# Performance work log

Measured on AMD Instinct MI355X. Metric: run time of the kernel, lower is better.

The kernel has to match this reference:

```python
import jax, jax.numpy as jnp
import numpy as np


def setup_inputs() -> dict:
    key = jax.random.key(0)
    ks = jax.random.split(key, 5)
    B, S, H = 4, 4096, 512
    std = 1.0 / np.sqrt(H)
    x = jax.random.normal(ks[0], (B, S, H), dtype=jnp.float32)
    relative_pos = jax.random.normal(ks[1], (B, S, H), dtype=jnp.float32)
    Wq = jax.random.normal(ks[2], (H, H), dtype=jnp.float32) * std
    Wk = jax.random.normal(ks[3], (H, H), dtype=jnp.float32) * std
    Wv = jax.random.normal(ks[4], (H, H), dtype=jnp.float32) * std
    bq = jnp.zeros((H,), dtype=jnp.float32)
    bk = jnp.zeros((H,), dtype=jnp.float32)
    bv = jnp.zeros((H,), dtype=jnp.float32)
    return {"x": x, "relative_pos": relative_pos, "Wq": Wq, "bq": bq,
            "Wk": Wk, "bk": bk, "Wv": Wv, "bv": bv}


def reference(x, relative_pos, Wq, bq, Wk, bk, Wv, bv):
    H = x.shape[-1]
    scale = jnp.sqrt(jnp.asarray(H, dtype=x.dtype))
    # torch Linear: y = x @ W^T + b
    Q = jnp.einsum('bsh,oh->bso', x, Wq) + bq
    K = jnp.einsum('bsh,oh->bso', x, Wk) + bk
    V = jnp.einsum('bsh,oh->bso', x, Wv) + bv
    Kr = jnp.einsum('bsh,oh->bso', relative_pos, Wk) + bk
    # two score terms, each [B,S,S]
    scores = (jnp.einsum('bqd,bkd->bqk', Q, K) +
              jnp.einsum('bqd,bkd->bqk', Q, Kr)) / scale
    weights = jax.nn.softmax(scores, axis=-1)
    return jnp.einsum('bqk,bkd->bqd', weights, V)
```

## Files before the change

### kernel.cpp

```cpp
#include <hip/hip_runtime.h>
#include <stdint.h>

typedef __attribute__((ext_vector_type(8))) short bf16x8;
typedef __attribute__((ext_vector_type(4))) float f32x4;

#define AS1 __attribute__((address_space(1)))
#define AS3 __attribute__((address_space(3)))

__device__ __forceinline__ void gl2lds16(const void* g, void* l) {
    __builtin_amdgcn_global_load_lds((const AS1 void*)g, (AS3 void*)l, 16, 0, 0);
}

__device__ __forceinline__ unsigned short f2bf(float f) {
    uint32_t u = __builtin_bit_cast(uint32_t, f);
    uint32_t r = (u + 0x7fffu + ((u >> 16) & 1u)) >> 16;
    return (unsigned short)r;
}

constexpr int S = 4096;
constexpr int H = 512;
constexpr size_t OFF_XB  = 0;
constexpr size_t OFF_SB  = 16777216;
constexpr size_t OFF_WQB = 33554432;
constexpr size_t OFF_WKB = 34078720;
constexpr size_t OFF_WVB = 34603008;
constexpr size_t OFF_BQK = 35127296;
constexpr size_t OFF_QB  = 35131392;
constexpr size_t OFF_K2B = OFF_QB  + 16777216;
constexpr size_t OFF_VTB = OFF_K2B + 16777216;
constexpr size_t OFF_PB  = OFF_VTB + 16777216;
constexpr size_t OFF_L   = OFF_PB  + 134217728;

__global__ __launch_bounds__(256) void prep_x(const float* __restrict__ x,
                                              const float* __restrict__ rp,
                                              unsigned short* __restrict__ xb,
                                              unsigned short* __restrict__ sb) {
    const int i = (blockIdx.x * 256 + threadIdx.x) * 4;
    float4 xv = *(const float4*)(x + i);
    float4 rv = *(const float4*)(rp + i);
    uint2 xo, so;
    xo.x = (uint32_t)f2bf(xv.x) | ((uint32_t)f2bf(xv.y) << 16);
    xo.y = (uint32_t)f2bf(xv.z) | ((uint32_t)f2bf(xv.w) << 16);
    so.x = (uint32_t)f2bf(xv.x + rv.x) | ((uint32_t)f2bf(xv.y + rv.y) << 16);
    so.y = (uint32_t)f2bf(xv.z + rv.z) | ((uint32_t)f2bf(xv.w + rv.w) << 16);
    *(uint2*)(xb + i) = xo;
    *(uint2*)(sb + i) = so;
}

__global__ __launch_bounds__(256) void prep_w(const float* __restrict__ wq,
                                              const float* __restrict__ wk,
                                              const float* __restrict__ wv,
                                              const float* __restrict__ bq,
                                              const float* __restrict__ bk,
                                              unsigned short* __restrict__ wqb,
                                              unsigned short* __restrict__ wkb,
                                              unsigned short* __restrict__ wvb,
                                              float* __restrict__ bqk,
                                              float* __restrict__ lrow) {
    const int t = blockIdx.x * 256 + threadIdx.x;
    const int i = t * 4;
    float4 q = *(const float4*)(wq + i);
    float4 k = *(const float4*)(wk + i);
    float4 v = *(const float4*)(wv + i);
    uint2 o;
    o.x = (uint32_t)f2bf(q.x) | ((uint32_t)f2bf(q.y) << 16);
    o.y = (uint32_t)f2bf(q.z) | ((uint32_t)f2bf(q.w) << 16);
    *(uint2*)(wqb + i) = o;
    o.x = (uint32_t)f2bf(k.x) | ((uint32_t)f2bf(k.y) << 16);
    o.y = (uint32_t)f2bf(k.z) | ((uint32_t)f2bf(k.w) << 16);
    *(uint2*)(wkb + i) = o;
    o.x = (uint32_t)f2bf(v.x) | ((uint32_t)f2bf(v.y) << 16);
    o.y = (uint32_t)f2bf(v.z) | ((uint32_t)f2bf(v.w) << 16);
    *(uint2*)(wvb + i) = o;
    if (t < 128) {
        *(float4*)(bqk + t * 4) = *(const float4*)(bq + t * 4);
    } else if (t < 256) {
        const int u = t - 128;
        float4 b = *(const float4*)(bk + u * 4);
        *(float4*)(bqk + 512 + u * 4) = make_float4(2.f * b.x, 2.f * b.y, 2.f * b.z, 2.f * b.w);
    }
    if (t < 4096) {
        *(float4*)(lrow + t * 4) = make_float4(0.f, 0.f, 0.f, 0.f);
    }
}

template <int MODE, int SWZ>
__global__ __launch_bounds__(256, 2)
void gemm_bt(const unsigned short* __restrict__ Abase,
             const unsigned short* __restrict__ Bbase,
             void* __restrict__ Cbase,
             int M, int N, int K,
             long long sAz, long long sBz, long long sCz,
             const float* __restrict__ bias_n, long long sBNz,
             const float* __restrict__ bias_m,
             float scale,
             float* __restrict__ rowdiv, long long sRz)
{
    int bx = blockIdx.x, by = blockIdx.y, bz = blockIdx.z;
    if (SWZ) {
        const int gx = gridDim.x, gy = gridDim.y;
        const int id  = bx + gx * (by + gridDim.y * bz);
        const int xcd = id & 7;
        const int k   = id >> 3;
        const int kg  = k / gx;
        bx = k - kg * gx;
        const int g = xcd + 8 * kg;
        const int gz = g / gy;
        by = g - gz * gy;
        bz = gz;
    }
    const int z = bz;
    const unsigned short* A  = Abase + (size_t)z * (size_t)sAz;
    const unsigned short* Bm = Bbase + (size_t)z * (size_t)sBz;
    const int bn = bx * 128;
    const int bm = by * 128;

    constexpr int SMEM_BYTES = (MODE == 2) ? (128 * 136 * 2) : (4 * 4096 * 2);
    __shared__ __align__(16) char smem[SMEM_BYTES];
    unsigned short* As = (unsigned short*)smem;
    unsigned short* Bs = (unsigned short*)(smem + 16384);

    const int tid  = threadIdx.x;
    const int wave = tid >> 6;
    const int lane = tid & 63;
    const int lm   = lane & 15;
    const int quad = lane >> 4;
    const int wm   = (wave >> 1) * 64;
    const int wn   = (wave & 1) * 64;

    const int r0 = tid >> 2;
    const int p0 = tid & 3;

    f32x4 acc[4][4] = {};

    for (int k0 = 0; k0 < K; k0 += 64) {
        __syncthreads();
        #pragma unroll
        for (int pp = 0; pp < 2; pp++) {
            const unsigned short* Ap = A  + (size_t)(bm + r0) * K + k0 + pp * 32 + p0 * 8;
            const unsigned short* Bp = Bm + (size_t)(bn + r0) * K + k0 + pp * 32 + p0 * 8;
            unsigned short* Asp = As + pp * 4096;
            unsigned short* Bsp = Bs + pp * 4096;
            gl2lds16(Ap,                    Asp + wave * 512);
            gl2lds16(Ap + (size_t)64 * K,   Asp + 2048 + wave * 512);
            gl2lds16(Bp,                    Bsp + wave * 512);
            gl2lds16(Bp + (size_t)64 * K,   Bsp + 2048 + wave * 512);
        }
        __syncthreads();

        #pragma unroll
        for (int pp = 0; pp < 2; pp++) {
            bf16x8 af[4], bfr[4];
            #pragma unroll
            for (int t = 0; t < 4; t++)
                af[t]  = *(const bf16x8*)(As + pp * 4096 + (wm + t * 16 + lm) * 32 + quad * 8);
            #pragma unroll
            for (int t = 0; t < 4; t++)
                bfr[t] = *(const bf16x8*)(Bs + pp * 4096 + (wn + t * 16 + lm) * 32 + quad * 8);
            #pragma unroll
            for (int mt = 0; mt < 4; mt++)
                #pragma unroll
                for (int nt = 0; nt < 4; nt++)
                    acc[mt][nt] = __builtin_amdgcn_mfma_f32_16x16x32_bf16(af[mt], bfr[nt], acc[mt][nt], 0, 0, 0);
        }
    }

    if (MODE == 0) {
        unsigned short* C = (unsigned short*)Cbase + (size_t)z * (size_t)sCz;
        const float* bn_ptr = bias_n ? bias_n + (size_t)z * (size_t)sBNz : nullptr;
        #pragma unroll
        for (int mt = 0; mt < 4; mt++) {
            #pragma unroll
            for (int i = 0; i < 4; i++) {
                const int row = bm + wm + mt * 16 + quad * 4 + i;
                const float badd = bias_m ? bias_m[row] : 0.0f;
                const size_t rb = (size_t)row * (size_t)N;
                #pragma unroll
                for (int nt = 0; nt < 4; nt++) {
                    const int col = bn + wn + nt * 16 + lm;
                    float v = acc[mt][nt][i] * scale + badd;
                    if (bn_ptr) v += bn_ptr[col];
                    C[rb + col] = f2bf(v);
                }
            }
        }
    } else if (MODE == 1) {
        float* C = (float*)Cbase + (size_t)z * (size_t)sCz;
        const float* rd = rowdiv + (size_t)z * (size_t)sRz;
        #pragma unroll
        for (int mt = 0; mt < 4; mt++) {
            #pragma unroll
            for (int i = 0; i < 4; i++) {
                const int row = bm + wm + mt * 16 + quad * 4 + i;
                const float inv = 1.0f / rd[row];
                const size_t rb = (size_t)row * (size_t)N;
                #pragma unroll
                for (int nt = 0; nt < 4; nt++) {
                    const int col = bn + wn + nt * 16 + lm;
                    C[rb + col] = acc[mt][nt][i] * inv;
                }
            }
        }
    } else {
        unsigned short* C = (unsigned short*)Cbase + (size_t)z * (size_t)sCz;
        float* lr = rowdiv + (size_t)z * (size_t)sRz;
        unsigned short* Ct = (unsigned short*)smem;
        __syncthreads();
        #pragma unroll
        for (int mt = 0; mt < 4; mt++) {
            #pragma unroll
            for (int i = 0; i < 4; i++) {
                const int r = wm + mt * 16 + quad * 4 + i;
                float rsum = 0.f;
                #pragma unroll
                for (int nt = 0; nt < 4; nt++) {
                    float p = __expf(acc[mt][nt][i] * scale);
                    rsum += p;
                    Ct[r * 136 + wn + nt * 16 + lm] = f2bf(p);
                }
                rsum += __shfl_xor(rsum, 1);
                rsum += __shfl_xor(rsum, 2);
                rsum += __shfl_xor(rsum, 4);
                rsum += __shfl_xor(rsum, 8);
                if (lm == 0) atomicAdd(lr + bm + r, rsum);
            }
        }
        __syncthreads();
        #pragma unroll
        for (int j = 0; j < 8; j++) {
            const int r   = (tid >> 4) + 16 * j;
            const int c16 = tid & 15;
            uint4 vv = *(const uint4*)(Ct + r * 136 + c16 * 8);
            *(uint4*)(C + (size_t)(bm + r) * (size_t)N + bn + c16 * 8) = vv;
        }
    }
}

extern "C" void kernel_launch(void* const* d_in, const int* in_sizes, int n_in,
                              void* d_out, int out_size, void* d_ws, size_t ws_size,
                              hipStream_t stream) {
    const float* x  = (const float*)d_in[0];
    const float* rp = (const float*)d_in[1];
    const float* Wq = (const float*)d_in[2];
    const float* bq = (const float*)d_in[3];
    const float* Wk = (const float*)d_in[4];
    const float* bk = (const float*)d_in[5];
    const float* Wv = (const float*)d_in[6];
    const float* bv = (const float*)d_in[7];

    char* ws = (char*)d_ws;
    unsigned short* xb  = (unsigned short*)(ws + OFF_XB);
    unsigned short* sb  = (unsigned short*)(ws + OFF_SB);
    unsigned short* wqb = (unsigned short*)(ws + OFF_WQB);
    unsigned short* wkb = (unsigned short*)(ws + OFF_WKB);
    unsigned short* wvb = (unsigned short*)(ws + OFF_WVB);
    float*          bqk = (float*)(ws + OFF_BQK);
    unsigned short* qb  = (unsigned short*)(ws + OFF_QB);
    unsigned short* k2b = (unsigned short*)(ws + OFF_K2B);
    unsigned short* vtb = (unsigned short*)(ws + OFF_VTB);
    unsigned short* pb  = (unsigned short*)(ws + OFF_PB);
    float*          lrow = (float*)(ws + OFF_L);

    prep_x<<<8192, 256, 0, stream>>>(x, rp, xb, sb);
    prep_w<<<256, 256, 0, stream>>>(Wq, Wk, Wv, bq, bk, wqb, wkb, wvb, bqk, lrow);

    gemm_bt<0, 1><<<dim3(4, 128, 2), 256, 0, stream>>>(
        xb, wqb, qb, 16384, 512, 512,
        8388608, 262144, 8388608,
        bqk, 512, nullptr, 1.0f, nullptr, 0);
    gemm_bt<0, 0><<<dim3(32, 4, 4), 256, 0, stream>>>(
        wvb, xb, vtb, 512, 4096, 512,
        0, (long long)S * H, (long long)S * H,
        nullptr, 0, bv, 1.0f, nullptr, 0);
    gemm_bt<2, 0><<<dim3(32, 32, 4), 256, 0, stream>>>(
        qb, k2b, pb, 4096, 4096, 512,
        (long long)S * H, (long long)S * H, (long long)S * S,
        nullptr, 0, nullptr, 0.044194173824159216f,
        lrow, 4096);
    gemm_bt<1, 1><<<dim3(4, 32, 4), 256, 0, stream>>>(
        pb, vtb, d_out, 4096, 512, 4096,
        (long long)S * S, (long long)S * H, (long long)S * H,
        nullptr, 0, nullptr, 1.0f, lrow, 4096);
}
```

Measured before the change: 347.5 us.

## Merge prep kernels, stage MODE-0 output via LDS, deepen PV K-panels

The two preprocessing kernels are merged into one launch that branches on block index. The projection GEMM epilogue (MODE 0) now writes its bf16 tile through LDS and stores coalesced 16-byte rows instead of scattered 2-byte stores. The final P·V GEMM loads four 32-wide K panels per sync instead of two, halving barrier count over its long K=4096 loop. The price is a larger LDS footprint for the PV kernel, which can limit occupancy.

```diff
diff --git a/kernel.cpp b/kernel.cpp
--- a/kernel.cpp
+++ b/kernel.cpp
@@ -31,60 +31,61 @@
 constexpr size_t OFF_PB  = OFF_VTB + 16777216;
 constexpr size_t OFF_L   = OFF_PB  + 134217728;
 
-__global__ __launch_bounds__(256) void prep_x(const float* __restrict__ x,
-                                              const float* __restrict__ rp,
-                                              unsigned short* __restrict__ xb,
-                                              unsigned short* __restrict__ sb) {
-    const int i = (blockIdx.x * 256 + threadIdx.x) * 4;
-    float4 xv = *(const float4*)(x + i);
-    float4 rv = *(const float4*)(rp + i);
-    uint2 xo, so;
-    xo.x = (uint32_t)f2bf(xv.x) | ((uint32_t)f2bf(xv.y) << 16);
-    xo.y = (uint32_t)f2bf(xv.z) | ((uint32_t)f2bf(xv.w) << 16);
-    so.x = (uint32_t)f2bf(xv.x + rv.x) | ((uint32_t)f2bf(xv.y + rv.y) << 16);
-    so.y = (uint32_t)f2bf(xv.z + rv.z) | ((uint32_t)f2bf(xv.w + rv.w) << 16);
-    *(uint2*)(xb + i) = xo;
-    *(uint2*)(sb + i) = so;
-}
-
-__global__ __launch_bounds__(256) void prep_w(const float* __restrict__ wq,
-                                              const float* __restrict__ wk,
-                                              const float* __restrict__ wv,
-                                              const float* __restrict__ bq,
-                                              const float* __restrict__ bk,
-                                              unsigned short* __restrict__ wqb,
-                                              unsigned short* __restrict__ wkb,
-                                              unsigned short* __restrict__ wvb,
-                                              float* __restrict__ bqk,
-                                              float* __restrict__ lrow) {
-    const int t = blockIdx.x * 256 + threadIdx.x;
-    const int i = t * 4;
-    float4 q = *(const float4*)(wq + i);
-    float4 k = *(const float4*)(wk + i);
-    float4 v = *(const float4*)(wv + i);
-    uint2 o;
-    o.x = (uint32_t)f2bf(q.x) | ((uint32_t)f2bf(q.y) << 16);
-    o.y = (uint32_t)f2bf(q.z) | ((uint32_t)f2bf(q.w) << 16);
-    *(uint2*)(wqb + i) = o;
-    o.x = (uint32_t)f2bf(k.x) | ((uint32_t)f2bf(k.y) << 16);
-    o.y = (uint32_t)f2bf(k.z) | ((uint32_t)f2bf(k.w) << 16);
-    *(uint2*)(wkb + i) = o;
-    o.x = (uint32_t)f2bf(v.x) | ((uint32_t)f2bf(v.y) << 16);
-    o.y = (uint32_t)f2bf(v.z) | ((uint32_t)f2bf(v.w) << 16);
-    *(uint2*)(wvb + i) = o;
-    if (t < 128) {
-        *(float4*)(bqk + t * 4) = *(const float4*)(bq + t * 4);
-    } else if (t < 256) {
-        const int u = t - 128;
-        float4 b = *(const float4*)(bk + u * 4);
-        *(float4*)(bqk + 512 + u * 4) = make_float4(2.f * b.x, 2.f * b.y, 2.f * b.z, 2.f * b.w);
-    }
-    if (t < 4096) {
-        *(float4*)(lrow + t * 4) = make_float4(0.f, 0.f, 0.f, 0.f);
-    }
-}
-
-template <int MODE, int SWZ>
+__global__ __launch_bounds__(256) void prep_all(const float* __restrict__ x,
+                                                const float* __restrict__ rp,
+                                                const float* __restrict__ wq,
+                                                const float* __restrict__ wk,
+                                                const float* __restrict__ wv,
+                                                const float* __restrict__ bq,
+                                                const float* __restrict__ bk,
+                                                unsigned short* __restrict__ xb,
+                                                unsigned short* __restrict__ sb,
+                                                unsigned short* __restrict__ wqb,
+                                                unsigned short* __restrict__ wkb,
+                                                unsigned short* __restrict__ wvb,
+                                                float* __restrict__ bqk,
+                                                float* __restrict__ lrow) {
+    if (blockIdx.x < 8192) {
+        const int i = (blockIdx.x * 256 + threadIdx.x) * 4;
+        float4 xv = *(const float4*)(x + i);
+        float4 rv = *(const float4*)(rp + i);
+        uint2 xo, so;
+        xo.x = (uint32_t)f2bf(xv.x) | ((uint32_t)f2bf(xv.y) << 16);
+        xo.y = (uint32_t)f2bf(xv.z) | ((uint32_t)f2bf(xv.w) << 16);
+        so.x = (uint32_t)f2bf(xv.x + rv.x) | ((uint32_t)f2bf(xv.y + rv.y) << 16);
+        so.y = (uint32_t)f2bf(xv.z + rv.z) | ((uint32_t)f2bf(xv.w + rv.w) << 16);
+        *(uint2*)(xb + i) = xo;
+        *(uint2*)(sb + i) = so;
+    } else {
+        const int t = (blockIdx.x - 8192) * 256 + threadIdx.x;
+        const int i = t * 4;
+        float4 q = *(const float4*)(wq + i);
+        float4 k = *(const float4*)(wk + i);
+        float4 v = *(const float4*)(wv + i);
+        uint2 o;
+        o.x = (uint32_t)f2bf(q.x) | ((uint32_t)f2bf(q.y) << 16);
+        o.y = (uint32_t)f2bf(q.z) | ((uint32_t)f2bf(q.w) << 16);
+        *(uint2*)(wqb + i) = o;
+        o.x = (uint32_t)f2bf(k.x) | ((uint32_t)f2bf(k.y) << 16);
+        o.y = (uint32_t)f2bf(k.z) | ((uint32_t)f2bf(k.w) << 16);
+        *(uint2*)(wkb + i) = o;
+        o.x = (uint32_t)f2bf(v.x) | ((uint32_t)f2bf(v.y) << 16);
+        o.y = (uint32_t)f2bf(v.z) | ((uint32_t)f2bf(v.w) << 16);
+        *(uint2*)(wvb + i) = o;
+        if (t < 128) {
+            *(float4*)(bqk + t * 4) = *(const float4*)(bq + t * 4);
+        } else if (t < 256) {
+            const int u = t - 128;
+            float4 b = *(const float4*)(bk + u * 4);
+            *(float4*)(bqk + 512 + u * 4) = make_float4(2.f * b.x, 2.f * b.y, 2.f * b.z, 2.f * b.w);
+        }
+        if (t < 4096) {
+            *(float4*)(lrow + t * 4) = make_float4(0.f, 0.f, 0.f, 0.f);
+        }
+    }
+}
+
+template <int MODE, int SWZ, int NPANEL>
 __global__ __launch_bounds__(256, 2)
 void gemm_bt(const unsigned short* __restrict__ Abase,
              const unsigned short* __restrict__ Bbase,
@@ -115,10 +116,12 @@
     const int bn = bx * 128;
     const int bm = by * 128;
 
-    constexpr int SMEM_BYTES = (MODE == 2) ? (128 * 136 * 2) : (4 * 4096 * 2);
+    constexpr int STAGE_BYTES = NPANEL * 16384;
+    constexpr int SMEM_BYTES = (MODE == 1) ? STAGE_BYTES
+                             : (STAGE_BYTES > 34816 ? STAGE_BYTES : 34816);
     __shared__ __align__(16) char smem[SMEM_BYTES];
     unsigned short* As = (unsigned short*)smem;
-    unsigned short* Bs = (unsigned short*)(smem + 16384);
+    unsigned short* Bs = (unsigned short*)(smem + NPANEL * 8192);
 
     const int tid  = threadIdx.x;
     const int wave = tid >> 6;
@@ -133,10 +136,10 @@
 
     f32x4 acc[4][4] = {};
 
-    for (int k0 = 0; k0 < K; k0 += 64) {
-        __syncthreads();
-        #pragma unroll
-        for (int pp = 0; pp < 2; pp++) {
+    for (int k0 = 0; k0 < K; k0 += 32 * NPANEL) {
+        __syncthreads();
+        #pragma unroll
+        for (int pp = 0; pp < NPANEL; pp++) {
             const unsigned short* Ap = A  + (size_t)(bm + r0) * K + k0 + pp * 32 + p0 * 8;
             const unsigned short* Bp = Bm + (size_t)(bn + r0) * K + k0 + pp * 32 + p0 * 8;
             unsigned short* Asp = As + pp * 4096;
@@ -149,7 +152,7 @@
         __syncthreads();
 
         #pragma unroll
-        for (int pp = 0; pp < 2; pp++) {
+        for (int pp = 0; pp < NPANEL; pp++) {
             bf16x8 af[4], bfr[4];
             #pragma unroll
             for (int t = 0; t < 4; t++)
@@ -165,26 +168,7 @@
         }
     }
 
-    if (MODE == 0) {
-        unsigned short* C = (unsigned short*)Cbase + (size_t)z * (size_t)sCz;
-        const float* bn_ptr = bias_n ? bias_n + (size_t)z * (size_t)sBNz : nullptr;
-        #pragma unroll
-        for (int mt = 0; mt < 4; mt++) {
-            #pragma unroll
-            for (int i = 0; i < 4; i++) {
-                const int row = bm + wm + mt * 16 + quad * 4 + i;
-                const float badd = bias_m ? bias_m[row] : 0.0f;
-                const size_t rb = (size_t)row * (size_t)N;
-                #pragma unroll
-                for (int nt = 0; nt < 4; nt++) {
-                    const int col = bn + wn + nt * 16 + lm;
-                    float v = acc[mt][nt][i] * scale + badd;
-                    if (bn_ptr) v += bn_ptr[col];
-                    C[rb + col] = f2bf(v);
-                }
-            }
-        }
-    } else if (MODE == 1) {
+    if (MODE == 1) {
         float* C = (float*)Cbase + (size_t)z * (size_t)sCz;
         const float* rd = rowdiv + (size_t)z * (size_t)sRz;
         #pragma unroll
@@ -203,7 +187,8 @@
         }
     } else {
         unsigned short* C = (unsigned short*)Cbase + (size_t)z * (size_t)sCz;
-        float* lr = rowdiv + (size_t)z * (size_t)sRz;
+        const float* bn_ptr = (MODE == 0 && bias_n) ? bias_n + (size_t)z * (size_t)sBNz : nullptr;
+        float* lr = (MODE == 2) ? rowdiv + (size_t)z * (size_t)sRz : nullptr;
         unsigned short* Ct = (unsigned short*)smem;
         __syncthreads();
         #pragma unroll
@@ -211,18 +196,29 @@
             #pragma unroll
             for (int i = 0; i < 4; i++) {
                 const int r = wm + mt * 16 + quad * 4 + i;
-                float rsum = 0.f;
-                #pragma unroll
-                for (int nt = 0; nt < 4; nt++) {
-                    float p = __expf(acc[mt][nt][i] * scale);
-                    rsum += p;
-                    Ct[r * 136 + wn + nt * 16 + lm] = f2bf(p);
+                if (MODE == 0) {
+                    const float badd = bias_m ? bias_m[bm + r] : 0.0f;
+                    #pragma unroll
+                    for (int nt = 0; nt < 4; nt++) {
+                        const int col = bn + wn + nt * 16 + lm;
+                        float v = acc[mt][nt][i] * scale + badd;
+                        if (bn_ptr) v += bn_ptr[col];
+                        Ct[r * 136 + wn + nt * 16 + lm] = f2bf(v);
+                    }
+                } else {
+                    float rsum = 0.f;
+                    #pragma unroll
+                    for (int nt = 0; nt < 4; nt++) {
+                        float p = __expf(acc[mt][nt][i] * scale);
+                        rsum += p;
+                        Ct[r * 136 + wn + nt * 16 + lm] = f2bf(p);
+                    }
+                    rsum += __shfl_xor(rsum, 1);
+                    rsum += __shfl_xor(rsum, 2);
+                    rsum += __shfl_xor(rsum, 4);
+                    rsum += __shfl_xor(rsum, 8);
+                    if (lm == 0) atomicAdd(lr + bm + r, rsum);
                 }
-                rsum += __shfl_xor(rsum, 1);
-                rsum += __shfl_xor(rsum, 2);
-                rsum += __shfl_xor(rsum, 4);
-                rsum += __shfl_xor(rsum, 8);
-                if (lm == 0) atomicAdd(lr + bm + r, rsum);
             }
         }
         __syncthreads();
@@ -261,23 +257,23 @@
     unsigned short* pb  = (unsigned short*)(ws + OFF_PB);
     float*          lrow = (float*)(ws + OFF_L);
 
-    prep_x<<<8192, 256, 0, stream>>>(x, rp, xb, sb);
-    prep_w<<<256, 256, 0, stream>>>(Wq, Wk, Wv, bq, bk, wqb, wkb, wvb, bqk, lrow);
-
-    gemm_bt<0, 1><<<dim3(4, 128, 2), 256, 0, stream>>>(
+    prep_all<<<8448, 256, 0, stream>>>(x, rp, Wq, Wk, Wv, bq, bk,
+                                       xb, sb, wqb, wkb, wvb, bqk, lrow);
+
+    gemm_bt<0, 1, 2><<<dim3(4, 128, 2), 256, 0, stream>>>(
         xb, wqb, qb, 16384, 512, 512,
         8388608, 262144, 8388608,
         bqk, 512, nullptr, 1.0f, nullptr, 0);
-    gemm_bt<0, 0><<<dim3(32, 4, 4), 256, 0, stream>>>(
+    gemm_bt<0, 0, 2><<<dim3(32, 4, 4), 256, 0, stream>>>(
         wvb, xb, vtb, 512, 4096, 512,
         0, (long long)S * H, (long long)S * H,
         nullptr, 0, bv, 1.0f, nullptr, 0);
-    gemm_bt<2, 0><<<dim3(32, 32, 4), 256, 0, stream>>>(
+    gemm_bt<2, 0, 2><<<dim3(32, 32, 4), 256, 0, stream>>>(
         qb, k2b, pb, 4096, 4096, 512,
         (long long)S * H, (long long)S * H, (long long)S * S,
         nullptr, 0, nullptr, 0.044194173824159216f,
         lrow, 4096);
-    gemm_bt<1, 1><<<dim3(4, 32, 4), 256, 0, stream>>>(
+    gemm_bt<1, 1, 4><<<dim3(4, 32, 4), 256, 0, stream>>>(
         pb, vtb, d_out, 4096, 512, 4096,
         (long long)S * S, (long long)S * H, (long long)S * H,
         nullptr, 0, nullptr, 1.0f, lrow, 4096);
```

After: 342.9 us. No clear change (-1.3%).
